# Performance work log

Measured on AMD Instinct MI355X. Metric: run time of the kernel, lower is better.

Reference implementation:

```python
import jax, jax.numpy as jnp
import numpy as np

G, N, H, L = 128, 32, 128, 6  # graphs, nodes/graph, hidden, conv layers


def _ln(x, g, b, eps=1e-5):
    m = jnp.mean(x, axis=-1, keepdims=True)
    v = jnp.var(x, axis=-1, keepdims=True)
    return (x - m) * jax.lax.rsqrt(v + eps) * g + b


def setup_inputs() -> dict:
    key = jax.random.key(0)
    ks = jax.random.split(key, 16)
    s = float(H) ** -0.5
    return {
        "x_idx": jax.random.randint(ks[0], (G * N,), 0, 32, dtype=jnp.int32),
        "ea_idx": jax.random.randint(ks[1], (G, N, N), 0, 16, dtype=jnp.int32),
        "tf_idx": jax.random.randint(ks[2], (G, N, N), 0, 16, dtype=jnp.int32),
        "adj": jax.random.randint(ks[3], (G, N, N), 0, 2, dtype=jnp.int32),
        "emb_x": 0.2 * jax.random.normal(ks[4], (32, H), dtype=jnp.float32),
        "emb_ea": 0.2 * jax.random.normal(ks[5], (16, H), dtype=jnp.float32),
        "emb_tf": 0.2 * jax.random.normal(ks[6], (16, H), dtype=jnp.float32),
        "W0": s * jax.random.normal(ks[7], (H, H), dtype=jnp.float32),
        "b0": jnp.zeros((H,), jnp.float32),
        "W1": s * jax.random.normal(ks[8], (H, H), dtype=jnp.float32),
        "b1": jnp.zeros((H,), jnp.float32),
        "Wc": s * jax.random.normal(ks[9], (L, H, H), dtype=jnp.float32),
        "bc": jnp.zeros((L, H), jnp.float32),
        "gc": jnp.ones((L, H), jnp.float32),
        "cc": jnp.zeros((L, H), jnp.float32),
        "Wp": s * jax.random.normal(ks[10], (H, H), dtype=jnp.float32),
        "bp": jnp.zeros((H,), jnp.float32),
        "gp": jnp.ones((H,), jnp.float32),
        "cp": jnp.zeros((H,), jnp.float32),
        "Wq1": s * jax.random.normal(ks[11], (H, H), dtype=jnp.float32),
        "bq1": jnp.zeros((H,), jnp.float32),
        "gq1": jnp.ones((H,), jnp.float32),
        "cq1": jnp.zeros((H,), jnp.float32),
        "Wq2": s * jax.random.normal(ks[12], (H, 1), dtype=jnp.float32),
        "bq2": jnp.zeros((1,), jnp.float32),
    }


def reference(x_idx, ea_idx, tf_idx, adj, emb_x, emb_ea, emb_tf,
              W0, b0, W1, b1, Wc, bc, gc, cc, Wp, bp, gp, cp,
              Wq1, bq1, gq1, cq1, Wq2, bq2):
    # InputEncoderSp: embedding lookups
    x = emb_x[x_idx]                                           # [G*N, H]
    Aval = emb_ea[ea_idx] * adj[..., None].astype(emb_ea.dtype)  # [G,N,N,H] masked edge emb
    # tupleinit: unpooling_fromdense1dim gathers lin(x) to tuple dims 0/1
    x0 = (x @ W0 + b0).reshape(G, N, H)
    x1 = (x @ W1 + b1).reshape(G, N, H)
    X = x0[:, :, None, :] * x1[:, None, :, :] * emb_tf[tf_idx]  # [G,N,N,H]
    for l in range(L):
        tX = jax.nn.relu(_ln(X @ Wc[l] + bc[l], gc[l], cc[l]))
        msg = jnp.einsum('gikh,gkjh->gijh', tX, Aval)          # sum_k tX[i,k]*A[k,j]
        X = X + msg
    # OpPoolingSubg2D('S','mean'): pool tuple dim 1 -> node features
    xs = jnp.mean(X, axis=2).reshape(G * N, H)                 # [G*N, H]
    xs = jax.nn.relu(_ln(xs @ Wp + bp, gp, cp))                # poolmlp
    hg = jnp.sum(xs.reshape(G, N, H), axis=1)                  # node->graph sum pool [G,H]
    # pred_lin: 2-layer MLP, tailact=False
    h = jax.nn.relu(_ln(hg @ Wq1 + bq1, gq1, cq1))
    return h @ Wq2 + bq2                                       # [G, num_tasks=1]
```

## Files before the change

### kernel.cpp

```cpp
#include <hip/hip_runtime.h>

#define G 128
#define N 32
#define H 128
#define L 6

typedef _Float16 half8 __attribute__((ext_vector_type(8)));
typedef float f32x4 __attribute__((ext_vector_type(4)));

__global__ __launch_bounds__(256) void k_packW(
    const float* __restrict__ Wc, _Float16* __restrict__ Wpk) {
  int l = blockIdx.x, tid = threadIdx.x;
  const float* W = Wc + (size_t)l * 16384;
  _Float16* hi = Wpk + (size_t)l * 32768;
  _Float16* lo = hi + 16384;
  for (int idx = tid; idx < 16384; idx += 256) {
    int k = idx >> 7, h = idx & 127;
    float v = W[idx];
    _Float16 a = (_Float16)v;
    hi[h * 128 + k] = a;
    lo[h * 128 + k] = (_Float16)(v - (float)a);
  }
}

__global__ __launch_bounds__(256) void k_codes(
    const int* __restrict__ ea_idx, const int* __restrict__ adj,
    unsigned char* __restrict__ codes) {
  int g = blockIdx.x, tid = threadIdx.x;
  int4 ev = ((const int4*)(ea_idx + (size_t)g * 1024))[tid];
  int4 av = ((const int4*)(adj   + (size_t)g * 1024))[tid];
  uchar4 c;
  c.x = av.x ? (unsigned char)ev.x : (unsigned char)16;
  c.y = av.y ? (unsigned char)ev.y : (unsigned char)16;
  c.z = av.z ? (unsigned char)ev.z : (unsigned char)16;
  c.w = av.w ? (unsigned char)ev.w : (unsigned char)16;
  ((uchar4*)(codes + (size_t)g * 1024))[tid] = c;
}

__global__ __launch_bounds__(256) void k_emb_mm(
    const float* __restrict__ emb_x,
    const float* __restrict__ W0, const float* __restrict__ b0, float* __restrict__ P0,
    const float* __restrict__ W1, const float* __restrict__ b1, float* __restrict__ P1) {
  const float* W = blockIdx.x ? W1 : W0;
  const float* b = blockIdx.x ? b1 : b0;
  float*       P = blockIdx.x ? P1 : P0;
  __shared__ float embs_t[128 * 32];
  int tid = threadIdx.x;
  {
    int i = tid & 31, k0 = (tid >> 5) * 16;
    const float* src = emb_x + i * 128 + k0;
#pragma unroll
    for (int m = 0; m < 16; m++) embs_t[(k0 + m) * 32 + i] = src[m];
  }
  __syncthreads();
  int i  = tid >> 3;
  int h0 = (tid & 7) * 16;
  float acc[16];
#pragma unroll
  for (int hh = 0; hh < 16; hh++) acc[hh] = b[h0 + hh];
  for (int k = 0; k < 128; k++) {
    float a = embs_t[k * 32 + i];
    const float4* wr = (const float4*)(W + k * 128 + h0);
    float4 w0 = wr[0], w1 = wr[1], w2 = wr[2], w3 = wr[3];
    acc[0]  += a * w0.x; acc[1]  += a * w0.y; acc[2]  += a * w0.z; acc[3]  += a * w0.w;
    acc[4]  += a * w1.x; acc[5]  += a * w1.y; acc[6]  += a * w1.z; acc[7]  += a * w1.w;
    acc[8]  += a * w2.x; acc[9]  += a * w2.y; acc[10] += a * w2.z; acc[11] += a * w2.w;
    acc[12] += a * w3.x; acc[13] += a * w3.y; acc[14] += a * w3.z; acc[15] += a * w3.w;
  }
  float4* dst = (float4*)(P + i * 128 + h0);
  dst[0] = make_float4(acc[0], acc[1], acc[2], acc[3]);
  dst[1] = make_float4(acc[4], acc[5], acc[6], acc[7]);
  dst[2] = make_float4(acc[8], acc[9], acc[10], acc[11]);
  dst[3] = make_float4(acc[12], acc[13], acc[14], acc[15]);
}

__global__ __launch_bounds__(256) void k_buildX(
    const int* __restrict__ x_idx, const int* __restrict__ tf_idx,
    const float* __restrict__ P0, const float* __restrict__ P1,
    const float* __restrict__ emb_tf, float* __restrict__ Xp) {
  int g = blockIdx.x >> 2, hb = (blockIdx.x & 3) * 32;
  int tid = threadIdx.x;
  __shared__ float x0t[32 * 32];
  __shared__ float x1t[32 * 32];
  __shared__ float etf[32 * 16];
  __shared__ int   tfs[1024];
  {
    int i = tid & 31, h0 = (tid >> 5) * 4;
    int r = x_idx[g * 32 + i];
    const float* s0 = P0 + r * 128 + hb + h0;
    const float* s1 = P1 + r * 128 + hb + h0;
#pragma unroll
    for (int m = 0; m < 4; m++) {
      x0t[(h0 + m) * 32 + i] = s0[m];
      x1t[(h0 + m) * 32 + i] = s1[m];
    }
  }
  if (tid < 32 * 16 / 2) {
    int t = tid & 15, h0 = (tid >> 4) * 2;
    const float* s = emb_tf + t * 128 + hb + h0;
    etf[(h0 + 0) * 16 + t] = s[0];
    etf[(h0 + 1) * 16 + t] = s[1];
  }
  ((int4*)tfs)[tid] = ((const int4*)(tf_idx + (size_t)g * 1024))[tid];
  __syncthreads();
  int i = tid >> 3, j0 = (tid & 7) * 4;
  int t0 = tfs[i * 32 + j0 + 0], t1 = tfs[i * 32 + j0 + 1];
  int t2 = tfs[i * 32 + j0 + 2], t3 = tfs[i * 32 + j0 + 3];
  float* outg = Xp + ((size_t)g << 17) + (size_t)hb * 1024;
  for (int h = 0; h < 32; h++) {
    float a = x0t[h * 32 + i];
    const float* x1r = x1t + h * 32;
    const float* er  = etf + h * 16;
    float4 v;
    v.x = a * x1r[j0 + 0] * er[t0];
    v.y = a * x1r[j0 + 1] * er[t1];
    v.z = a * x1r[j0 + 2] * er[t2];
    v.w = a * x1r[j0 + 3] * er[t3];
    *(float4*)(outg + h * 1024 + tid * 4) = v;
  }
}

__global__ __launch_bounds__(256, 4) void k_conv_mlp(
    const float* __restrict__ Xp, const _Float16* __restrict__ Wpk,
    const float* __restrict__ bcl, const float* __restrict__ gcl,
    const float* __restrict__ ccl, float* __restrict__ tXp) {
  int g = blockIdx.x >> 3, qb = blockIdx.x & 7;
  int tid = threadIdx.x;
  int lane = tid & 63, wv = tid >> 6;
  int x = lane & 15, quad = lane >> 4;

  f32x4 acc[2][8];
#pragma unroll
  for (int hh = 0; hh < 8; hh++) {
    float4 b4 = *(const float4*)(bcl + hh * 16 + quad * 4);
    f32x4 bi; bi[0] = b4.x; bi[1] = b4.y; bi[2] = b4.z; bi[3] = b4.w;
    acc[0][hh] = bi; acc[1][hh] = bi;
  }

  const float* Xg = Xp + ((size_t)g << 17) + qb * 128 + wv * 32 + x;
  const _Float16* Wlo = Wpk + 16384;

#pragma unroll
  for (int c = 0; c < 4; c++) {
    int kb = c * 32 + quad * 8;
    half8 bh[2], bl[2];
#pragma unroll
    for (int pt = 0; pt < 2; pt++) {
      const float* xc = Xg + pt * 16 + (size_t)kb * 1024;
#pragma unroll
      for (int i = 0; i < 8; i++) {
        float v = xc[(size_t)i * 1024];
        _Float16 hi = (_Float16)v;
        bh[pt][i] = hi;
        bl[pt][i] = (_Float16)(v - (float)hi);
      }
    }
#pragma unroll
    for (int hh = 0; hh < 8; hh++) {
      int wo = (hh * 16 + x) * 128 + kb;
      half8 ah = *(const half8*)(Wpk + wo);
      half8 al = *(const half8*)(Wlo + wo);
#pragma unroll
      for (int pt = 0; pt < 2; pt++) {
        acc[pt][hh] = __builtin_amdgcn_mfma_f32_16x16x32_f16(ah, bh[pt], acc[pt][hh], 0, 0, 0);
        acc[pt][hh] = __builtin_amdgcn_mfma_f32_16x16x32_f16(ah, bl[pt], acc[pt][hh], 0, 0, 0);
        acc[pt][hh] = __builtin_amdgcn_mfma_f32_16x16x32_f16(al, bh[pt], acc[pt][hh], 0, 0, 0);
      }
    }
  }

  float gm[2], gr[2];
#pragma unroll
  for (int pt = 0; pt < 2; pt++) {
    float s = 0.f;
#pragma unroll
    for (int hh = 0; hh < 8; hh++)
#pragma unroll
      for (int r = 0; r < 4; r++) s += acc[pt][hh][r];
    s += __shfl_xor(s, 16);
    s += __shfl_xor(s, 32);
    float m = s * (1.f / 128.f);
    float qv = 0.f;
#pragma unroll
    for (int hh = 0; hh < 8; hh++)
#pragma unroll
      for (int r = 0; r < 4; r++) { float d = acc[pt][hh][r] - m; qv += d * d; }
    qv += __shfl_xor(qv, 16);
    qv += __shfl_xor(qv, 32);
    gm[pt] = m;
    gr[pt] = rsqrtf(qv * (1.f / 128.f) + 1e-5f);
  }
  int pbase = qb * 128 + wv * 32;
#pragma unroll
  for (int hh = 0; hh < 8; hh++) {
    float4 g4 = *(const float4*)(gcl + hh * 16 + quad * 4);
    float4 c4 = *(const float4*)(ccl + hh * 16 + quad * 4);
    float ga[4] = {g4.x, g4.y, g4.z, g4.w};
    float ca[4] = {c4.x, c4.y, c4.z, c4.w};
#pragma unroll
    for (int r = 0; r < 4; r++) {
      int h = hh * 16 + quad * 4 + r;
      float* dst = tXp + (((size_t)(g * 128 + h)) << 10) + pbase + x;
#pragma unroll
      for (int pt = 0; pt < 2; pt++) {
        float v = (acc[pt][hh][r] - gm[pt]) * gr[pt] * ga[r] + ca[r];
        dst[pt * 16] = fmaxf(v, 0.f);
      }
    }
  }
}

template <bool LAST>
__global__ __launch_bounds__(256, 4) void k_conv_msg(
    const float* __restrict__ tXp, const unsigned char* __restrict__ codes,
    const float* __restrict__ emb_ea,
    float* __restrict__ Xp, float* __restrict__ xs) {
  int g  = blockIdx.x >> 4;
  int hb = (blockIdx.x & 15) * 8;
  int tid = threadIdx.x, wv = tid >> 6, lane = tid & 63;
  __shared__ unsigned char c8[1024];
  __shared__ float eacs[8][20];
  __shared__ __align__(16) float tXs[4][32 * 36];
  __shared__ __align__(16) float As[4][32 * 36];
  ((uchar4*)c8)[tid] = ((const uchar4*)(codes + (size_t)g * 1024))[tid];
  if (tid < 128) {
    int hh = tid >> 4, e = tid & 15;
    eacs[hh][e] = emb_ea[e * 128 + hb + hh];
  }
  if (tid >= 128 && tid < 136) eacs[tid - 128][16] = 0.f;
  __syncthreads();
  int i0 = (lane >> 3) * 4, j0 = (lane & 7) * 4;
  float* tw = tXs[wv];
  float* aw = As[wv];
#pragma unroll 1
  for (int pl = 0; pl < 2; pl++) {
    int hh = wv * 2 + pl;
    int h  = hb + hh;
    const float4* tp = (const float4*)(tXp + (((size_t)(g * 128 + h)) << 10));
#pragma unroll
    for (int m = 0; m < 4; m++) {
      int f = lane + 64 * m;
      float4 v = tp[f];
      *(float4*)&tw[(f >> 3) * 36 + (f & 7) * 4] = v;
    }
#pragma unroll
    for (int m = 0; m < 4; m++) {
      int qd = lane + 64 * m;
      uchar4 cc = ((const uchar4*)c8)[qd];
      float4 a;
      a.x = eacs[hh][cc.x]; a.y = eacs[hh][cc.y];
      a.z = eacs[hh][cc.z]; a.w = eacs[hh][cc.w];
      *(float4*)&aw[(qd >> 3) * 36 + (qd & 7) * 4] = a;
    }
    float4 a0 = {0, 0, 0, 0}, a1 = a0, a2 = a0, a3 = a0;
#pragma unroll
    for (int kb = 0; kb < 8; kb++) {
      int k4 = kb * 4;
      float4 t0 = *(const float4*)&tw[(i0 + 0) * 36 + k4];
      float4 t1 = *(const float4*)&tw[(i0 + 1) * 36 + k4];
      float4 t2 = *(const float4*)&tw[(i0 + 2) * 36 + k4];
      float4 t3 = *(const float4*)&tw[(i0 + 3) * 36 + k4];
      float4 b0 = *(const float4*)&aw[(k4 + 0) * 36 + j0];
      float4 b1 = *(const float4*)&aw[(k4 + 1) * 36 + j0];
      float4 b2 = *(const float4*)&aw[(k4 + 2) * 36 + j0];
      float4 b3 = *(const float4*)&aw[(k4 + 3) * 36 + j0];
      a0.x += t0.x * b0.x; a0.y += t0.x * b0.y; a0.z += t0.x * b0.z; a0.w += t0.x * b0.w;
      a0.x += t0.y * b1.x; a0.y += t0.y * b1.y; a0.z += t0.y * b1.z; a0.w += t0.y * b1.w;
      a0.x += t0.z * b2.x; a0.y += t0.z * b2.y; a0.z += t0.z * b2.z; a0.w += t0.z * b2.w;
      a0.x += t0.w * b3.x; a0.y += t0.w * b3.y; a0.z += t0.w * b3.z; a0.w += t0.w * b3.w;
      a1.x += t1.x * b0.x; a1.y += t1.x * b0.y; a1.z += t1.x * b0.z; a1.w += t1.x * b0.w;
      a1.x += t1.y * b1.x; a1.y += t1.y * b1.y; a1.z += t1.y * b1.z; a1.w += t1.y * b1.w;
      a1.x += t1.z * b2.x; a1.y += t1.z * b2.y; a1.z += t1.z * b2.z; a1.w += t1.z * b2.w;
      a1.x += t1.w * b3.x; a1.y += t1.w * b3.y; a1.z += t1.w * b3.z; a1.w += t1.w * b3.w;
      a2.x += t2.x * b0.x; a2.y += t2.x * b0.y; a2.z += t2.x * b0.z; a2.w += t2.x * b0.w;
      a2.x += t2.y * b1.x; a2.y += t2.y * b1.y; a2.z += t2.y * b1.z; a2.w += t2.y * b1.w;
      a2.x += t2.z * b2.x; a2.y += t2.z * b2.y; a2.z += t2.z * b2.z; a2.w += t2.z * b2.w;
      a2.x += t2.w * b3.x; a2.y += t2.w * b3.y; a2.z += t2.w * b3.z; a2.w += t2.w * b3.w;
      a3.x += t3.x * b0.x; a3.y += t3.x * b0.y; a3.z += t3.x * b0.z; a3.w += t3.x * b0.w;
      a3.x += t3.y * b1.x; a3.y += t3.y * b1.y; a3.z += t3.y * b1.z; a3.w += t3.y * b1.w;
      a3.x += t3.z * b2.x; a3.y += t3.z * b2.y; a3.z += t3.z * b2.z; a3.w += t3.z * b2.w;
      a3.x += t3.w * b3.x; a3.y += t3.w * b3.y; a3.z += t3.w * b3.z; a3.w += t3.w * b3.w;
    }
    float* xr = Xp + (((size_t)(g * 128 + h)) << 10);
    float4* r0 = (float4*)&xr[(i0 + 0) * 32 + j0];
    float4* r1 = (float4*)&xr[(i0 + 1) * 32 + j0];
    float4* r2 = (float4*)&xr[(i0 + 2) * 32 + j0];
    float4* r3 = (float4*)&xr[(i0 + 3) * 32 + j0];
    float4 x0 = *r0, x1 = *r1, x2 = *r2, x3 = *r3;
    x0.x += a0.x; x0.y += a0.y; x0.z += a0.z; x0.w += a0.w;
    x1.x += a1.x; x1.y += a1.y; x1.z += a1.z; x1.w += a1.w;
    x2.x += a2.x; x2.y += a2.y; x2.z += a2.z; x2.w += a2.w;
    x3.x += a3.x; x3.y += a3.y; x3.z += a3.z; x3.w += a3.w;
    if (!LAST) {
      *r0 = x0; *r1 = x1; *r2 = x2; *r3 = x3;
    } else {
      float s0 = (x0.x + x0.y) + (x0.z + x0.w);
      float s1 = (x1.x + x1.y) + (x1.z + x1.w);
      float s2 = (x2.x + x2.y) + (x2.z + x2.w);
      float s3 = (x3.x + x3.y) + (x3.z + x3.w);
      s0 += __shfl_xor(s0, 1); s0 += __shfl_xor(s0, 2); s0 += __shfl_xor(s0, 4);
      s1 += __shfl_xor(s1, 1); s1 += __shfl_xor(s1, 2); s1 += __shfl_xor(s1, 4);
      s2 += __shfl_xor(s2, 1); s2 += __shfl_xor(s2, 2); s2 += __shfl_xor(s2, 4);
      s3 += __shfl_xor(s3, 1); s3 += __shfl_xor(s3, 2); s3 += __shfl_xor(s3, 4);
      if ((lane & 7) == 0) {
        float* xo = xs + ((size_t)(g * 32 + i0)) * 128 + h;
        xo[0]   = s0 * (1.f / 32.f);
        xo[128] = s1 * (1.f / 32.f);
        xo[256] = s2 * (1.f / 32.f);
        xo[384] = s3 * (1.f / 32.f);
      }
    }
  }
}

__global__ __launch_bounds__(256) void k_tail2(
    const float* __restrict__ xs,
    const float* __restrict__ Wp, const float* __restrict__ bp,
    const float* __restrict__ gp, const float* __restrict__ cp,
    const float* __restrict__ Wq1, const float* __restrict__ bq1,
    const float* __restrict__ gq1, const float* __restrict__ cq1,
    const float* __restrict__ Wq2, const float* __restrict__ bq2,
    float* __restrict__ out) {
  int g = blockIdx.x, tid = threadIdx.x;
  __shared__ float xsl[32 * 132];
  __shared__ float y_s[32 * 132];
  __shared__ float red8[32][9];
  __shared__ float hg_s[128];
  __shared__ float q_s[128];
  __shared__ float stat[2];
  {
    const float4* src = (const float4*)(xs + (size_t)g * 4096);
#pragma unroll
    for (int m = 0; m < 4; m++) {
      int f = m * 256 + tid;
      int row = f >> 5, col = (f & 31) * 4;
      *(float4*)&xsl[row * 132 + col] = src[f];
    }
  }
  __syncthreads();
  int i_ = tid >> 3, ht = tid & 7, h0 = ht * 16;
  float acc[16];
#pragma unroll
  for (int hh = 0; hh < 16; hh++) acc[hh] = bp[h0 + hh];
  for (int k = 0; k < 128; k++) {
    float a = xsl[i_ * 132 + k];
    const float4* wr = (const float4*)(Wp + k * 128 + h0);
    float4 w0 = wr[0], w1 = wr[1], w2 = wr[2], w3 = wr[3];
    acc[0]  += a * w0.x; acc[1]  += a * w0.y; acc[2]  += a * w0.z; acc[3]  += a * w0.w;
    acc[4]  += a * w1.x; acc[5]  += a * w1.y; acc[6]  += a * w1.z; acc[7]  += a * w1.w;
    acc[8]  += a * w2.x; acc[9]  += a * w2.y; acc[10] += a * w2.z; acc[11] += a * w2.w;
    acc[12] += a * w3.x; acc[13] += a * w3.y; acc[14] += a * w3.z; acc[15] += a * w3.w;
  }
  {
    float s = 0.f;
#pragma unroll
    for (int hh = 0; hh < 16; hh++) s += acc[hh];
    red8[i_][ht] = s;
  }
  __syncthreads();
  float m = 0.f;
#pragma unroll
  for (int t = 0; t < 8; t++) m += red8[i_][t];
  m *= (1.f / 128.f);
  __syncthreads();
  {
    float q = 0.f;
#pragma unroll
    for (int hh = 0; hh < 16; hh++) { float d = acc[hh] - m; q += d * d; }
    red8[i_][ht] = q;
  }
  __syncthreads();
  float v = 0.f;
#pragma unroll
  for (int t = 0; t < 8; t++) v += red8[i_][t];
  float r = rsqrtf(v * (1.f / 128.f) + 1e-5f);
#pragma unroll
  for (int hh = 0; hh < 16; hh++) {
    int hcol = h0 + hh;
    y_s[i_ * 132 + hcol] = fmaxf((acc[hh] - m) * r * gp[hcol] + cp[hcol], 0.f);
  }
  __syncthreads();
  if (tid < 128) {
    float sh = 0.f;
#pragma unroll
    for (int ii = 0; ii < 32; ii++) sh += y_s[ii * 132 + tid];
    hg_s[tid] = sh;
  }
  __syncthreads();
  if (tid < 128) {
    float a = bq1[tid];
    for (int k = 0; k < 128; k++) a += hg_s[k] * Wq1[k * 128 + tid];
    q_s[tid] = a;
  }
  __syncthreads();
  if (tid < 64) {
    float s2 = q_s[tid] + q_s[tid + 64];
    s2 += __shfl_xor(s2, 1);  s2 += __shfl_xor(s2, 2);  s2 += __shfl_xor(s2, 4);
    s2 += __shfl_xor(s2, 8);  s2 += __shfl_xor(s2, 16); s2 += __shfl_xor(s2, 32);
    if (tid == 0) stat[0] = s2 * (1.f / 128.f);
  }
  __syncthreads();
  float mq = stat[0];
  if (tid < 64) {
    float d0 = q_s[tid] - mq, d1 = q_s[tid + 64] - mq;
    float v2 = d0 * d0 + d1 * d1;
    v2 += __shfl_xor(v2, 1);  v2 += __shfl_xor(v2, 2);  v2 += __shfl_xor(v2, 4);
    v2 += __shfl_xor(v2, 8);  v2 += __shfl_xor(v2, 16); v2 += __shfl_xor(v2, 32);
    if (tid == 0) stat[1] = rsqrtf(v2 * (1.f / 128.f) + 1e-5f);
  }
  __syncthreads();
  float rq = stat[1];
  if (tid < 64) {
    float a0 = fmaxf((q_s[tid]      - mq) * rq * gq1[tid]      + cq1[tid],      0.f) * Wq2[tid];
    float a1 = fmaxf((q_s[tid + 64] - mq) * rq * gq1[tid + 64] + cq1[tid + 64], 0.f) * Wq2[tid + 64];
    float t = a0 + a1;
    t += __shfl_xor(t, 1);  t += __shfl_xor(t, 2);  t += __shfl_xor(t, 4);
    t += __shfl_xor(t, 8);  t += __shfl_xor(t, 16); t += __shfl_xor(t, 32);
    if (tid == 0) out[g] = t + bq2[0];
  }
}

extern "C" void kernel_launch(void* const* d_in, const int* in_sizes, int n_in,
                              void* d_out, int out_size, void* d_ws, size_t ws_size,
                              hipStream_t stream) {
  const int*   x_idx  = (const int*)d_in[0];
  const int*   ea_idx = (const int*)d_in[1];
  const int*   tf_idx = (const int*)d_in[2];
  const int*   adj    = (const int*)d_in[3];
  const float* emb_x  = (const float*)d_in[4];
  const float* emb_ea = (const float*)d_in[5];
  const float* emb_tf = (const float*)d_in[6];
  const float* W0  = (const float*)d_in[7];
  const float* b0  = (const float*)d_in[8];
  const float* W1  = (const float*)d_in[9];
  const float* b1  = (const float*)d_in[10];
  const float* Wc  = (const float*)d_in[11];
  const float* bc  = (const float*)d_in[12];
  const float* gc  = (const float*)d_in[13];
  const float* cc  = (const float*)d_in[14];
  const float* Wp  = (const float*)d_in[15];
  const float* bp  = (const float*)d_in[16];
  const float* gp  = (const float*)d_in[17];
  const float* cp  = (const float*)d_in[18];
  const float* Wq1 = (const float*)d_in[19];
  const float* bq1 = (const float*)d_in[20];
  const float* gq1 = (const float*)d_in[21];
  const float* cq1 = (const float*)d_in[22];
  const float* Wq2 = (const float*)d_in[23];
  const float* bq2 = (const float*)d_in[24];
  float* out = (float*)d_out;

  float* ws  = (float*)d_ws;
  float* Xp  = ws;
  float* tXp = ws + (size_t)16777216;
  float* P0  = ws + (size_t)33554432;
  float* P1  = P0 + 4096;
  float* xs  = ws + (size_t)33562624;
  _Float16* Wpk = (_Float16*)(ws + (size_t)34086912);
  unsigned char* codes = (unsigned char*)(ws + (size_t)34185216);

  k_packW<<<6, 256, 0, stream>>>(Wc, Wpk);
  k_codes<<<G, 256, 0, stream>>>(ea_idx, adj, codes);
  k_emb_mm<<<2, 256, 0, stream>>>(emb_x, W0, b0, P0, W1, b1, P1);
  k_buildX<<<G * 4, 256, 0, stream>>>(x_idx, tf_idx, P0, P1, emb_tf, Xp);
  for (int l = 0; l < L; l++) {
    k_conv_mlp<<<G * 8, 256, 0, stream>>>(Xp, Wpk + (size_t)l * 32768,
                                          bc + l * H, gc + l * H, cc + l * H, tXp);
    if (l < L - 1)
      k_conv_msg<false><<<G * 16, 256, 0, stream>>>(tXp, codes, emb_ea, Xp, xs);
    else
      k_conv_msg<true><<<G * 16, 256, 0, stream>>>(tXp, codes, emb_ea, Xp, xs);
  }
  k_tail2<<<G, 256, 0, stream>>>(xs, Wp, bp, gp, cp, Wq1, bq1, gq1, cq1, Wq2, bq2, out);
}
```

Before: 681.8 us.

## Store tX as fp16 and compute message SpMM with MFMA split-precision

The intermediate tX buffer is now written in fp16, halving its write and read traffic. The message kernel replaces the scalar FP32 32x32 matmul with 32x32x16 MFMA, using a hi/lo fp16 split of the edge embeddings, with one head per wave and twice as many blocks. The MLP kernel also stages X tiles through shared memory with coalesced float4 loads instead of strided scalar global loads. Storing tX in fp16 drops the low-order bits of the activations, which costs some accuracy.

```diff
diff --git a/kernel.cpp b/kernel.cpp
--- a/kernel.cpp
+++ b/kernel.cpp
@@ -7,6 +7,7 @@
 
 typedef _Float16 half8 __attribute__((ext_vector_type(8)));
 typedef float f32x4 __attribute__((ext_vector_type(4)));
+typedef float f32x16 __attribute__((ext_vector_type(16)));
 
 __global__ __launch_bounds__(256) void k_packW(
     const float* __restrict__ Wc, _Float16* __restrict__ Wpk) {
@@ -123,11 +124,12 @@
 __global__ __launch_bounds__(256, 4) void k_conv_mlp(
     const float* __restrict__ Xp, const _Float16* __restrict__ Wpk,
     const float* __restrict__ bcl, const float* __restrict__ gcl,
-    const float* __restrict__ ccl, float* __restrict__ tXp) {
+    const float* __restrict__ ccl, _Float16* __restrict__ tXh) {
   int g = blockIdx.x >> 3, qb = blockIdx.x & 7;
   int tid = threadIdx.x;
   int lane = tid & 63, wv = tid >> 6;
   int x = lane & 15, quad = lane >> 4;
+  __shared__ __align__(16) float Xs[32 * 132];
 
   f32x4 acc[2][8];
 #pragma unroll
@@ -137,24 +139,33 @@
     acc[0][hh] = bi; acc[1][hh] = bi;
   }
 
-  const float* Xg = Xp + ((size_t)g << 17) + qb * 128 + wv * 32 + x;
+  const float* Xg = Xp + ((size_t)g << 17) + qb * 128;
   const _Float16* Wlo = Wpk + 16384;
-
-#pragma unroll
+  int srow = tid >> 3, scol = (tid & 7) * 16;
+
+#pragma unroll 1
   for (int c = 0; c < 4; c++) {
-    int kb = c * 32 + quad * 8;
+    float4 st[4];
+    const float* src = Xg + (size_t)(c * 32 + srow) * 1024 + scol;
+#pragma unroll
+    for (int m = 0; m < 4; m++) st[m] = ((const float4*)src)[m];
+    __syncthreads();
+#pragma unroll
+    for (int m = 0; m < 4; m++) *(float4*)&Xs[srow * 132 + scol + 4 * m] = st[m];
+    __syncthreads();
     half8 bh[2], bl[2];
 #pragma unroll
     for (int pt = 0; pt < 2; pt++) {
-      const float* xc = Xg + pt * 16 + (size_t)kb * 1024;
+      int p = wv * 32 + pt * 16 + x;
 #pragma unroll
       for (int i = 0; i < 8; i++) {
-        float v = xc[(size_t)i * 1024];
+        float v = Xs[(quad * 8 + i) * 132 + p];
         _Float16 hi = (_Float16)v;
         bh[pt][i] = hi;
         bl[pt][i] = (_Float16)(v - (float)hi);
       }
     }
+    int kb = c * 32 + quad * 8;
 #pragma unroll
     for (int hh = 0; hh < 8; hh++) {
       int wo = (hh * 16 + x) * 128 + kb;
@@ -200,115 +211,76 @@
 #pragma unroll
     for (int r = 0; r < 4; r++) {
       int h = hh * 16 + quad * 4 + r;
-      float* dst = tXp + (((size_t)(g * 128 + h)) << 10) + pbase + x;
+      _Float16* dst = tXh + (((size_t)(g * 128 + h)) << 10) + pbase + x;
 #pragma unroll
       for (int pt = 0; pt < 2; pt++) {
         float v = (acc[pt][hh][r] - gm[pt]) * gr[pt] * ga[r] + ca[r];
-        dst[pt * 16] = fmaxf(v, 0.f);
+        dst[pt * 16] = (_Float16)fmaxf(v, 0.f);
       }
     }
   }
 }
 
 template <bool LAST>
-__global__ __launch_bounds__(256, 4) void k_conv_msg(
-    const float* __restrict__ tXp, const unsigned char* __restrict__ codes,
+__global__ __launch_bounds__(256) void k_conv_msg(
+    const _Float16* __restrict__ tXh, const unsigned char* __restrict__ codes,
     const float* __restrict__ emb_ea,
     float* __restrict__ Xp, float* __restrict__ xs) {
-  int g  = blockIdx.x >> 4;
-  int hb = (blockIdx.x & 15) * 8;
+  int g   = blockIdx.x >> 5;
+  int hb4 = (blockIdx.x & 31) * 4;
   int tid = threadIdx.x, wv = tid >> 6, lane = tid & 63;
   __shared__ unsigned char c8[1024];
-  __shared__ float eacs[8][20];
-  __shared__ __align__(16) float tXs[4][32 * 36];
-  __shared__ __align__(16) float As[4][32 * 36];
+  __shared__ _Float16 ehi[4][20];
+  __shared__ _Float16 elo[4][20];
   ((uchar4*)c8)[tid] = ((const uchar4*)(codes + (size_t)g * 1024))[tid];
-  if (tid < 128) {
+  if (tid < 64) {
     int hh = tid >> 4, e = tid & 15;
-    eacs[hh][e] = emb_ea[e * 128 + hb + hh];
-  }
-  if (tid >= 128 && tid < 136) eacs[tid - 128][16] = 0.f;
-  __syncthreads();
-  int i0 = (lane >> 3) * 4, j0 = (lane & 7) * 4;
-  float* tw = tXs[wv];
-  float* aw = As[wv];
-#pragma unroll 1
-  for (int pl = 0; pl < 2; pl++) {
-    int hh = wv * 2 + pl;
-    int h  = hb + hh;
-    const float4* tp = (const float4*)(tXp + (((size_t)(g * 128 + h)) << 10));
-#pragma unroll
-    for (int m = 0; m < 4; m++) {
-      int f = lane + 64 * m;
-      float4 v = tp[f];
-      *(float4*)&tw[(f >> 3) * 36 + (f & 7) * 4] = v;
-    }
-#pragma unroll
-    for (int m = 0; m < 4; m++) {
-      int qd = lane + 64 * m;
-      uchar4 cc = ((const uchar4*)c8)[qd];
-      float4 a;
-      a.x = eacs[hh][cc.x]; a.y = eacs[hh][cc.y];
-      a.z = eacs[hh][cc.z]; a.w = eacs[hh][cc.w];
-      *(float4*)&aw[(qd >> 3) * 36 + (qd & 7) * 4] = a;
-    }
-    float4 a0 = {0, 0, 0, 0}, a1 = a0, a2 = a0, a3 = a0;
-#pragma unroll
-    for (int kb = 0; kb < 8; kb++) {
-      int k4 = kb * 4;
-      float4 t0 = *(const float4*)&tw[(i0 + 0) * 36 + k4];
-      float4 t1 = *(const float4*)&tw[(i0 + 1) * 36 + k4];
-      float4 t2 = *(const float4*)&tw[(i0 + 2) * 36 + k4];
-      float4 t3 = *(const float4*)&tw[(i0 + 3) * 36 + k4];
-      float4 b0 = *(const float4*)&aw[(k4 + 0) * 36 + j0];
-      float4 b1 = *(const float4*)&aw[(k4 + 1) * 36 + j0];
-      float4 b2 = *(const float4*)&aw[(k4 + 2) * 36 + j0];
-      float4 b3 = *(const float4*)&aw[(k4 + 3) * 36 + j0];
-      a0.x += t0.x * b0.x; a0.y += t0.x * b0.y; a0.z += t0.x * b0.z; a0.w += t0.x * b0.w;
-      a0.x += t0.y * b1.x; a0.y += t0.y * b1.y; a0.z += t0.y * b1.z; a0.w += t0.y * b1.w;
-      a0.x += t0.z * b2.x; a0.y += t0.z * b2.y; a0.z += t0.z * b2.z; a0.w += t0.z * b2.w;
-      a0.x += t0.w * b3.x; a0.y += t0.w * b3.y; a0.z += t0.w * b3.z; a0.w += t0.w * b3.w;
-      a1.x += t1.x * b0.x; a1.y += t1.x * b0.y; a1.z += t1.x * b0.z; a1.w += t1.x * b0.w;
-      a1.x += t1.y * b1.x; a1.y += t1.y * b1.y; a1.z += t1.y * b1.z; a1.w += t1.y * b1.w;
-      a1.x += t1.z * b2.x; a1.y += t1.z * b2.y; a1.z += t1.z * b2.z; a1.w += t1.z * b2.w;
-      a1.x += t1.w * b3.x; a1.y += t1.w * b3.y; a1.z += t1.w * b3.z; a1.w += t1.w * b3.w;
-      a2.x += t2.x * b0.x; a2.y += t2.x * b0.y; a2.z += t2.x * b0.z; a2.w += t2.x * b0.w;
-      a2.x += t2.y * b1.x; a2.y += t2.y * b1.y; a2.z += t2.y * b1.z; a2.w += t2.y * b1.w;
-      a2.x += t2.z * b2.x; a2.y += t2.z * b2.y; a2.z += t2.z * b2.z; a2.w += t2.z * b2.w;
-      a2.x += t2.w * b3.x; a2.y += t2.w * b3.y; a2.z += t2.w * b3.z; a2.w += t2.w * b3.w;
-      a3.x += t3.x * b0.x; a3.y += t3.x * b0.y; a3.z += t3.x * b0.z; a3.w += t3.x * b0.w;
-      a3.x += t3.y * b1.x; a3.y += t3.y * b1.y; a3.z += t3.y * b1.z; a3.w += t3.y * b1.w;
-      a3.x += t3.z * b2.x; a3.y += t3.z * b2.y; a3.z += t3.z * b2.z; a3.w += t3.z * b2.w;
-      a3.x += t3.w * b3.x; a3.y += t3.w * b3.y; a3.z += t3.w * b3.z; a3.w += t3.w * b3.w;
-    }
-    float* xr = Xp + (((size_t)(g * 128 + h)) << 10);
-    float4* r0 = (float4*)&xr[(i0 + 0) * 32 + j0];
-    float4* r1 = (float4*)&xr[(i0 + 1) * 32 + j0];
-    float4* r2 = (float4*)&xr[(i0 + 2) * 32 + j0];
-    float4* r3 = (float4*)&xr[(i0 + 3) * 32 + j0];
-    float4 x0 = *r0, x1 = *r1, x2 = *r2, x3 = *r3;
-    x0.x += a0.x; x0.y += a0.y; x0.z += a0.z; x0.w += a0.w;
-    x1.x += a1.x; x1.y += a1.y; x1.z += a1.z; x1.w += a1.w;
-    x2.x += a2.x; x2.y += a2.y; x2.z += a2.z; x2.w += a2.w;
-    x3.x += a3.x; x3.y += a3.y; x3.z += a3.z; x3.w += a3.w;
-    if (!LAST) {
-      *r0 = x0; *r1 = x1; *r2 = x2; *r3 = x3;
-    } else {
-      float s0 = (x0.x + x0.y) + (x0.z + x0.w);
-      float s1 = (x1.x + x1.y) + (x1.z + x1.w);
-      float s2 = (x2.x + x2.y) + (x2.z + x2.w);
-      float s3 = (x3.x + x3.y) + (x3.z + x3.w);
-      s0 += __shfl_xor(s0, 1); s0 += __shfl_xor(s0, 2); s0 += __shfl_xor(s0, 4);
-      s1 += __shfl_xor(s1, 1); s1 += __shfl_xor(s1, 2); s1 += __shfl_xor(s1, 4);
-      s2 += __shfl_xor(s2, 1); s2 += __shfl_xor(s2, 2); s2 += __shfl_xor(s2, 4);
-      s3 += __shfl_xor(s3, 1); s3 += __shfl_xor(s3, 2); s3 += __shfl_xor(s3, 4);
-      if ((lane & 7) == 0) {
-        float* xo = xs + ((size_t)(g * 32 + i0)) * 128 + h;
-        xo[0]   = s0 * (1.f / 32.f);
-        xo[128] = s1 * (1.f / 32.f);
-        xo[256] = s2 * (1.f / 32.f);
-        xo[384] = s3 * (1.f / 32.f);
-      }
+    float v = emb_ea[e * 128 + hb4 + hh];
+    _Float16 hi = (_Float16)v;
+    ehi[hh][e] = hi;
+    elo[hh][e] = (_Float16)(v - (float)hi);
+  } else if (tid < 68) {
+    ehi[tid - 64][16] = (_Float16)0.f;
+    elo[tid - 64][16] = (_Float16)0.f;
+  }
+  __syncthreads();
+
+  int h = hb4 + wv;
+  int col = lane & 31, khalf = lane >> 5;
+  const _Float16* tp = tXh + (((size_t)(g * 128 + h)) << 10) + col * 32 + khalf * 8;
+  half8 a0 = *(const half8*)tp;
+  half8 a1 = *(const half8*)(tp + 16);
+  half8 bh0, bl0, bh1, bl1;
+  int kb = khalf * 8;
+#pragma unroll
+  for (int j = 0; j < 8; j++) {
+    int c0 = c8[(kb + j) * 32 + col];
+    int c1 = c8[(16 + kb + j) * 32 + col];
+    bh0[j] = ehi[wv][c0]; bl0[j] = elo[wv][c0];
+    bh1[j] = ehi[wv][c1]; bl1[j] = elo[wv][c1];
+  }
+  f32x16 acc = {};
+  acc = __builtin_amdgcn_mfma_f32_32x32x16_f16(a0, bh0, acc, 0, 0, 0);
+  acc = __builtin_amdgcn_mfma_f32_32x32x16_f16(a0, bl0, acc, 0, 0, 0);
+  acc = __builtin_amdgcn_mfma_f32_32x32x16_f16(a1, bh1, acc, 0, 0, 0);
+  acc = __builtin_amdgcn_mfma_f32_32x32x16_f16(a1, bl1, acc, 0, 0, 0);
+
+  float* xr = Xp + (((size_t)(g * 128 + h)) << 10);
+  if (!LAST) {
+#pragma unroll
+    for (int reg = 0; reg < 16; reg++) {
+      int row = (reg & 3) + 8 * (reg >> 2) + 4 * khalf;
+      float* p = xr + row * 32 + col;
+      *p += acc[reg];
+    }
+  } else {
+#pragma unroll
+    for (int reg = 0; reg < 16; reg++) {
+      int row = (reg & 3) + 8 * (reg >> 2) + 4 * khalf;
+      float s = xr[row * 32 + col] + acc[reg];
+      s += __shfl_xor(s, 1);  s += __shfl_xor(s, 2);  s += __shfl_xor(s, 4);
+      s += __shfl_xor(s, 8);  s += __shfl_xor(s, 16);
+      if (col == 0) xs[((size_t)(g * 32 + row)) * 128 + h] = s * (1.f / 32.f);
     }
   }
 }
@@ -452,7 +424,7 @@
 
   float* ws  = (float*)d_ws;
   float* Xp  = ws;
-  float* tXp = ws + (size_t)16777216;
+  _Float16* tXh = (_Float16*)(ws + (size_t)16777216);
   float* P0  = ws + (size_t)33554432;
   float* P1  = P0 + 4096;
   float* xs  = ws + (size_t)33562624;
@@ -465,11 +437,11 @@
   k_buildX<<<G * 4, 256, 0, stream>>>(x_idx, tf_idx, P0, P1, emb_tf, Xp);
   for (int l = 0; l < L; l++) {
     k_conv_mlp<<<G * 8, 256, 0, stream>>>(Xp, Wpk + (size_t)l * 32768,
-                                          bc + l * H, gc + l * H, cc + l * H, tXp);
+                                          bc + l * H, gc + l * H, cc + l * H, tXh);
     if (l < L - 1)
-      k_conv_msg<false><<<G * 16, 256, 0, stream>>>(tXp, codes, emb_ea, Xp, xs);
+      k_conv_msg<false><<<G * 32, 256, 0, stream>>>(tXh, codes, emb_ea, Xp, xs);
     else
-      k_conv_msg<true><<<G * 16, 256, 0, stream>>>(tXp, codes, emb_ea, Xp, xs);
+      k_conv_msg<true><<<G * 32, 256, 0, stream>>>(tXh, codes, emb_ea, Xp, xs);
   }
   k_tail2<<<G, 256, 0, stream>>>(xs, Wp, bp, gp, cp, Wq1, bq1, gq1, cq1, Wq2, bq2, out);
 }
```

Result: slower. 730.4 us (+7.1%).

## Store MLP intermediate as packed fp16 pairs and halve per-block tile

Applied to the files above, without the earlier changes.

The conv MLP kernel now writes its ReLU(LN) output as fp16, packing two adjacent hidden channels into one 32-bit word. This halves the tX intermediate traffic between the MLP and message kernels, and the message kernel unpacks the half it needs. The MLP kernel also processes 16 tuple rows per wave instead of 32, doubling the grid and raising the occupancy hint from 4 to 6 blocks. Storing tX in fp16 loses precision on the activations that feed the message aggregation, though each message wave still reads a full uint4 row of packed data.

```diff
diff --git a/kernel.cpp b/kernel.cpp
--- a/kernel.cpp
+++ b/kernel.cpp
@@ -7,6 +7,14 @@
 
 typedef _Float16 half8 __attribute__((ext_vector_type(8)));
 typedef float f32x4 __attribute__((ext_vector_type(4)));
+
+__device__ inline unsigned short f16_bits(_Float16 h) {
+  union { _Float16 f; unsigned short u; } c; c.f = h; return c.u;
+}
+__device__ inline float half_of(unsigned d, int idx) {
+  union { unsigned u; _Float16 h[2]; } c; c.u = d;
+  return (float)c.h[idx];
+}
 
 __global__ __launch_bounds__(256) void k_packW(
     const float* __restrict__ Wc, _Float16* __restrict__ Wpk) {
@@ -120,77 +128,67 @@
   }
 }
 
-__global__ __launch_bounds__(256, 4) void k_conv_mlp(
+__global__ __launch_bounds__(256, 6) void k_conv_mlp(
     const float* __restrict__ Xp, const _Float16* __restrict__ Wpk,
     const float* __restrict__ bcl, const float* __restrict__ gcl,
-    const float* __restrict__ ccl, float* __restrict__ tXp) {
-  int g = blockIdx.x >> 3, qb = blockIdx.x & 7;
+    const float* __restrict__ ccl, unsigned* __restrict__ tXh2) {
+  int g = blockIdx.x >> 4, qb = blockIdx.x & 15;
   int tid = threadIdx.x;
   int lane = tid & 63, wv = tid >> 6;
   int x = lane & 15, quad = lane >> 4;
 
-  f32x4 acc[2][8];
+  f32x4 acc[8];
 #pragma unroll
   for (int hh = 0; hh < 8; hh++) {
     float4 b4 = *(const float4*)(bcl + hh * 16 + quad * 4);
     f32x4 bi; bi[0] = b4.x; bi[1] = b4.y; bi[2] = b4.z; bi[3] = b4.w;
-    acc[0][hh] = bi; acc[1][hh] = bi;
-  }
-
-  const float* Xg = Xp + ((size_t)g << 17) + qb * 128 + wv * 32 + x;
+    acc[hh] = bi;
+  }
+
+  int base = qb * 64 + wv * 16;
+  const float* Xg = Xp + ((size_t)g << 17) + base + x;
   const _Float16* Wlo = Wpk + 16384;
 
 #pragma unroll
   for (int c = 0; c < 4; c++) {
     int kb = c * 32 + quad * 8;
-    half8 bh[2], bl[2];
-#pragma unroll
-    for (int pt = 0; pt < 2; pt++) {
-      const float* xc = Xg + pt * 16 + (size_t)kb * 1024;
-#pragma unroll
-      for (int i = 0; i < 8; i++) {
-        float v = xc[(size_t)i * 1024];
-        _Float16 hi = (_Float16)v;
-        bh[pt][i] = hi;
-        bl[pt][i] = (_Float16)(v - (float)hi);
-      }
+    half8 bh, bl;
+#pragma unroll
+    for (int i = 0; i < 8; i++) {
+      float v = Xg[(size_t)(kb + i) * 1024];
+      _Float16 hi = (_Float16)v;
+      bh[i] = hi;
+      bl[i] = (_Float16)(v - (float)hi);
     }
 #pragma unroll
     for (int hh = 0; hh < 8; hh++) {
       int wo = (hh * 16 + x) * 128 + kb;
       half8 ah = *(const half8*)(Wpk + wo);
       half8 al = *(const half8*)(Wlo + wo);
-#pragma unroll
-      for (int pt = 0; pt < 2; pt++) {
-        acc[pt][hh] = __builtin_amdgcn_mfma_f32_16x16x32_f16(ah, bh[pt], acc[pt][hh], 0, 0, 0);
-        acc[pt][hh] = __builtin_amdgcn_mfma_f32_16x16x32_f16(ah, bl[pt], acc[pt][hh], 0, 0, 0);
-        acc[pt][hh] = __builtin_amdgcn_mfma_f32_16x16x32_f16(al, bh[pt], acc[pt][hh], 0, 0, 0);
-      }
-    }
-  }
-
-  float gm[2], gr[2];
-#pragma unroll
-  for (int pt = 0; pt < 2; pt++) {
-    float s = 0.f;
-#pragma unroll
-    for (int hh = 0; hh < 8; hh++)
-#pragma unroll
-      for (int r = 0; r < 4; r++) s += acc[pt][hh][r];
-    s += __shfl_xor(s, 16);
-    s += __shfl_xor(s, 32);
-    float m = s * (1.f / 128.f);
-    float qv = 0.f;
-#pragma unroll
-    for (int hh = 0; hh < 8; hh++)
-#pragma unroll
-      for (int r = 0; r < 4; r++) { float d = acc[pt][hh][r] - m; qv += d * d; }
-    qv += __shfl_xor(qv, 16);
-    qv += __shfl_xor(qv, 32);
-    gm[pt] = m;
-    gr[pt] = rsqrtf(qv * (1.f / 128.f) + 1e-5f);
-  }
-  int pbase = qb * 128 + wv * 32;
+      acc[hh] = __builtin_amdgcn_mfma_f32_16x16x32_f16(ah, bh, acc[hh], 0, 0, 0);
+      acc[hh] = __builtin_amdgcn_mfma_f32_16x16x32_f16(ah, bl, acc[hh], 0, 0, 0);
+      acc[hh] = __builtin_amdgcn_mfma_f32_16x16x32_f16(al, bh, acc[hh], 0, 0, 0);
+    }
+  }
+
+  float s = 0.f;
+#pragma unroll
+  for (int hh = 0; hh < 8; hh++)
+#pragma unroll
+    for (int r = 0; r < 4; r++) s += acc[hh][r];
+  s += __shfl_xor(s, 16);
+  s += __shfl_xor(s, 32);
+  float m = s * (1.f / 128.f);
+  float qv = 0.f;
+#pragma unroll
+  for (int hh = 0; hh < 8; hh++)
+#pragma unroll
+    for (int r = 0; r < 4; r++) { float d = acc[hh][r] - m; qv += d * d; }
+  qv += __shfl_xor(qv, 16);
+  qv += __shfl_xor(qv, 32);
+  float rs = rsqrtf(qv * (1.f / 128.f) + 1e-5f);
+
+  unsigned* outg = tXh2 + (size_t)(g * 64) * 1024 + base + x;
 #pragma unroll
   for (int hh = 0; hh < 8; hh++) {
     float4 g4 = *(const float4*)(gcl + hh * 16 + quad * 4);
@@ -198,21 +196,20 @@
     float ga[4] = {g4.x, g4.y, g4.z, g4.w};
     float ca[4] = {c4.x, c4.y, c4.z, c4.w};
 #pragma unroll
-    for (int r = 0; r < 4; r++) {
-      int h = hh * 16 + quad * 4 + r;
-      float* dst = tXp + (((size_t)(g * 128 + h)) << 10) + pbase + x;
-#pragma unroll
-      for (int pt = 0; pt < 2; pt++) {
-        float v = (acc[pt][hh][r] - gm[pt]) * gr[pt] * ga[r] + ca[r];
-        dst[pt * 16] = fmaxf(v, 0.f);
-      }
+    for (int rp = 0; rp < 2; rp++) {
+      float v0 = fmaxf((acc[hh][2 * rp]     - m) * rs * ga[2 * rp]     + ca[2 * rp],     0.f);
+      float v1 = fmaxf((acc[hh][2 * rp + 1] - m) * rs * ga[2 * rp + 1] + ca[2 * rp + 1], 0.f);
+      unsigned u = (unsigned)f16_bits((_Float16)v0) |
+                   ((unsigned)f16_bits((_Float16)v1) << 16);
+      int hp = (hh * 16 + quad * 4 + 2 * rp) >> 1;
+      outg[(size_t)hp * 1024] = u;
     }
   }
 }
 
 template <bool LAST>
 __global__ __launch_bounds__(256, 4) void k_conv_msg(
-    const float* __restrict__ tXp, const unsigned char* __restrict__ codes,
+    const unsigned* __restrict__ tXh2, const unsigned char* __restrict__ codes,
     const float* __restrict__ emb_ea,
     float* __restrict__ Xp, float* __restrict__ xs) {
   int g  = blockIdx.x >> 4;
@@ -232,15 +229,18 @@
   int i0 = (lane >> 3) * 4, j0 = (lane & 7) * 4;
   float* tw = tXs[wv];
   float* aw = As[wv];
+  const unsigned* prow = tXh2 + (size_t)(g * 64 + (hb >> 1) + wv) * 1024;
 #pragma unroll 1
   for (int pl = 0; pl < 2; pl++) {
     int hh = wv * 2 + pl;
     int h  = hb + hh;
-    const float4* tp = (const float4*)(tXp + (((size_t)(g * 128 + h)) << 10));
 #pragma unroll
     for (int m = 0; m < 4; m++) {
       int f = lane + 64 * m;
-      float4 v = tp[f];
+      uint4 d = ((const uint4*)prow)[f];
+      float4 v;
+      v.x = half_of(d.x, pl); v.y = half_of(d.y, pl);
+      v.z = half_of(d.z, pl); v.w = half_of(d.w, pl);
       *(float4*)&tw[(f >> 3) * 36 + (f & 7) * 4] = v;
     }
 #pragma unroll
@@ -452,24 +452,24 @@
 
   float* ws  = (float*)d_ws;
   float* Xp  = ws;
-  float* tXp = ws + (size_t)16777216;
-  float* P0  = ws + (size_t)33554432;
+  unsigned* tXh2 = (unsigned*)(ws + (size_t)16777216);
+  float* P0  = ws + (size_t)25165824;
   float* P1  = P0 + 4096;
-  float* xs  = ws + (size_t)33562624;
-  _Float16* Wpk = (_Float16*)(ws + (size_t)34086912);
-  unsigned char* codes = (unsigned char*)(ws + (size_t)34185216);
+  float* xs  = ws + (size_t)25174016;
+  _Float16* Wpk = (_Float16*)(ws + (size_t)25698304);
+  unsigned char* codes = (unsigned char*)(ws + (size_t)25796608);
 
   k_packW<<<6, 256, 0, stream>>>(Wc, Wpk);
   k_codes<<<G, 256, 0, stream>>>(ea_idx, adj, codes);
   k_emb_mm<<<2, 256, 0, stream>>>(emb_x, W0, b0, P0, W1, b1, P1);
   k_buildX<<<G * 4, 256, 0, stream>>>(x_idx, tf_idx, P0, P1, emb_tf, Xp);
   for (int l = 0; l < L; l++) {
-    k_conv_mlp<<<G * 8, 256, 0, stream>>>(Xp, Wpk + (size_t)l * 32768,
-                                          bc + l * H, gc + l * H, cc + l * H, tXp);
+    k_conv_mlp<<<G * 16, 256, 0, stream>>>(Xp, Wpk + (size_t)l * 32768,
+                                           bc + l * H, gc + l * H, cc + l * H, tXh2);
     if (l < L - 1)
-      k_conv_msg<false><<<G * 16, 256, 0, stream>>>(tXp, codes, emb_ea, Xp, xs);
+      k_conv_msg<false><<<G * 16, 256, 0, stream>>>(tXh2, codes, emb_ea, Xp, xs);
     else
-      k_conv_msg<true><<<G * 16, 256, 0, stream>>>(tXp, codes, emb_ea, Xp, xs);
+      k_conv_msg<true><<<G * 16, 256, 0, stream>>>(tXh2, codes, emb_ea, Xp, xs);
   }
   k_tail2<<<G, 256, 0, stream>>>(xs, Wp, bp, gp, cp, Wq1, bq1, gq1, cq1, Wq2, bq2, out);
 }
```

Measured after the change: 848.0 us. +24.4%, slower.
